# Kernel tuning notes

Hardware: AMD Instinct MI355X
Metric: run time of the kernel (lower is better)

Reference implementation:

```python
import jax, jax.numpy as jnp
import numpy as np

N = 100000
E_RAND = 800000
IN_D, HID_D, OUT_D = 128, 64, 64
PROP_STEP = 8
ATTN_AFT = PROP_STEP // 2  # attention applied after this many prop steps
LAM = 1.0
ALP = 1.0 / (LAM + 1.0)    # alp=0 in init -> DGL auto-sets 1/(lam+1)
TAU = 0.2
P_RHO = 1.0
T_UP = -1.0                # T<=0 -> no upper threshold


def setup_inputs() -> dict:
    key = jax.random.key(0)
    k1, k2, k3, k4, k5 = jax.random.split(key, 5)
    loops = jnp.arange(N)
    src = jnp.concatenate([jax.random.randint(k1, (E_RAND,), 0, N), loops]).astype(jnp.int32)
    dst = jnp.concatenate([jax.random.randint(k2, (E_RAND,), 0, N), loops]).astype(jnp.int32)
    feat = jax.random.normal(k3, (N, IN_D), jnp.float32)
    # xavier_normal init, zero bias (as in MLP.reset_params)
    W_bef = jax.random.normal(k4, (IN_D, HID_D), jnp.float32) * np.float32(np.sqrt(2.0 / (IN_D + HID_D)))
    b_bef = jnp.zeros((HID_D,), jnp.float32)
    W_aft = jax.random.normal(k5, (HID_D, OUT_D), jnp.float32) * np.float32(np.sqrt(2.0 / (HID_D + OUT_D)))
    b_aft = jnp.zeros((OUT_D,), jnp.float32)
    return {"feat": feat, "W_bef": W_bef, "b_bef": b_bef, "W_aft": W_aft, "b_aft": b_aft, "src": src, "dst": dst}


def _ax(src, dst, w, X):
    # Y = A X with per-edge weights: scatter-add of w_e * X[src_e] into dst_e
    return jax.ops.segment_sum(X[src] * w[:, None], dst, num_segments=N)


def _attention(src, dst, Y):
    hs, hd = Y[src], Y[dst]  # [E, d]
    w = jnp.sum(hs * hs, -1) + jnp.sum(hd * hd, -1) - 2.0 * jnp.sum(hs * hd, -1)  # ||h_u - h_v||^2
    w = jax.nn.relu(w) + 1e-7
    w = jnp.power(w, 1.0 - 0.5 * P_RHO)
    w = jnp.maximum(w, TAU)  # lower threshold tau (in-place clamp in torch)
    if T_UP > 0:
        w = jnp.where(w > T_UP, jnp.inf, w)
    w = 1.0 / w + 1e-9
    deg = jax.ops.segment_sum(w, dst, num_segments=N)  # copy_e -> sum per dst node
    return w, deg


def _prop(src, dst, w, deg, Y, X):
    dt = LAM * deg + (1.0 - LAM)
    nrm = jnp.power(dt, -0.5)[:, None]
    py = nrm * _ax(src, dst, w, nrm * Y)
    return (1.0 - ALP) * Y + ALP * LAM * py + ALP * (X / dt[:, None])


def reference(feat, W_bef, b_bef, W_aft, b_aft, src, dst):
    X = feat @ W_bef + b_bef  # mlp_bef: single Linear(input_d, hidden_d)
    w = jnp.ones(src.shape[0], feat.dtype)  # initial edge weights = 1
    deg = jax.ops.segment_sum(w, dst, num_segments=N)  # in-degrees
    Y = X
    for k in range(PROP_STEP):
        Y = _prop(src, dst, w, deg, Y, X)
        if k == ATTN_AFT - 1:
            w, deg = _attention(src, dst, Y)
    # mlp_aft: init_activate=True (relu; norm='none', dropout=0) then Linear(hidden_d, output_d)
    return jax.nn.relu(Y) @ W_aft + b_aft
```

## Files before the change

### kernel.cpp

```cpp
#include <hip/hip_runtime.h>
#include <math.h>

#define IN_D 128
#define HID 64

typedef unsigned short ushort_t;
typedef unsigned int uint_t;

static __device__ __forceinline__ ushort_t f2bf(float f) {
    uint_t x = __float_as_uint(f);
    uint_t r = x + 0x7fffu + ((x >> 16) & 1u);
    return (ushort_t)(r >> 16);
}
static __device__ __forceinline__ float bf2f(ushort_t u) {
    return __uint_as_float(((uint_t)u) << 16);
}


__global__ void zero1_kernel(int* a, int n) {
    int i = blockIdx.x * blockDim.x + threadIdx.x;
    if (i < n) a[i] = 0;
}

__global__ void hist_kernel(const int* __restrict__ dst, int E, int* __restrict__ cnt) {
    int e = blockIdx.x * blockDim.x + threadIdx.x;
    if (e < E) atomicAdd(&cnt[dst[e]], 1);
}

__global__ void scan1_kernel(int* __restrict__ cnt, int N,
                             int* __restrict__ row_ptr, int* __restrict__ blocksum,
                             float* __restrict__ nrm, float* __restrict__ invdt) {
    __shared__ int sm[1024];
    int i = blockIdx.x * 1024 + threadIdx.x;
    int v = (i < N) ? cnt[i] : 0;
    if (i < N) {
        cnt[i] = 0;
        float d = (float)v;
        nrm[i] = 1.0f / sqrtf(d);
        invdt[i] = 1.0f / d;
    }
    sm[threadIdx.x] = v;
    __syncthreads();
    for (int off = 1; off < 1024; off <<= 1) {
        int t = (threadIdx.x >= off) ? sm[threadIdx.x - off] : 0;
        __syncthreads();
        sm[threadIdx.x] += t;
        __syncthreads();
    }
    if (i < N) row_ptr[i + 1] = sm[threadIdx.x];
    if (threadIdx.x == 1023) blocksum[blockIdx.x] = sm[1023];
}

__global__ void scan2_kernel(int* __restrict__ blocksum, int nb) {
    __shared__ int sm[1024];
    int v = (threadIdx.x < nb) ? blocksum[threadIdx.x] : 0;
    sm[threadIdx.x] = v;
    __syncthreads();
    for (int off = 1; off < 1024; off <<= 1) {
        int t = (threadIdx.x >= off) ? sm[threadIdx.x - off] : 0;
        __syncthreads();
        sm[threadIdx.x] += t;
        __syncthreads();
    }
    if (threadIdx.x < nb) blocksum[threadIdx.x] = sm[threadIdx.x] - v;
}

__global__ void scan3_kernel(int* __restrict__ row_ptr, int N, const int* __restrict__ blocksum) {
    int i = blockIdx.x * 1024 + threadIdx.x;
    if (i < N) row_ptr[i + 1] += blocksum[blockIdx.x];
    if (i == 0) row_ptr[0] = 0;
}

__global__ void scatter_kernel(const int* __restrict__ src, const int* __restrict__ dst, int E,
                               const int* __restrict__ row_ptr, int* __restrict__ cursor,
                               const float* __restrict__ nrm,
                               int* __restrict__ src_perm, int* __restrict__ dst_perm,
                               float* __restrict__ coef) {
    int e = blockIdx.x * blockDim.x + threadIdx.x;
    if (e < E) {
        int d = dst[e];
        int s = src[e];
        int pos = row_ptr[d] + atomicAdd(&cursor[d], 1);
        src_perm[pos] = s;
        dst_perm[pos] = d;
        coef[pos] = nrm[s];
    }
}

__global__ void coef_kernel(const int* __restrict__ src_perm, const float* __restrict__ w_perm,
                            const float* __restrict__ nrm, int E, float* __restrict__ coef) {
    int e = blockIdx.x * blockDim.x + threadIdx.x;
    if (e < E) coef[e] = w_perm[e] * nrm[src_perm[e]];
}


__global__ __launch_bounds__(256) void prop_kernel(
    const float* __restrict__ Yin, const ushort_t* __restrict__ Ybf,
    const float* __restrict__ X,
    const int* __restrict__ row_ptr, const int* __restrict__ src_perm,
    const float* __restrict__ coef, const float* __restrict__ nrm,
    const float* __restrict__ invdt, int N,
    float* __restrict__ Yout, ushort_t* __restrict__ Yout_bf) {
    int wave = (blockIdx.x * blockDim.x + threadIdx.x) >> 6;
    int lane = threadIdx.x & 63;
    if (wave >= N) return;
    int r0 = row_ptr[wave], r1 = row_ptr[wave + 1];
    float acc = 0.0f;
    for (int jb = r0; jb < r1; jb += 64) {
        int m = r1 - jb;
        if (m > 64) m = 64;
        int sv = 0;
        float cv = 0.0f;
        if (lane < m) { sv = src_perm[jb + lane]; cv = coef[jb + lane]; }
        for (int t = 0; t < m; t += 16) {
            float v[16], c[16];
            #pragma unroll
            for (int u = 0; u < 16; ++u) {
                int idx = t + u;
                int active = idx < m;
                if (!active) idx = 0;
                int s = __shfl(sv, idx, 64);
                float cc = __shfl(cv, idx, 64);
                c[u] = active ? cc : 0.0f;
                v[u] = bf2f(Ybf[(size_t)s * HID + lane]);
            }
            #pragma unroll
            for (int u = 0; u < 16; ++u) acc = fmaf(c[u], v[u], acc);
        }
    }
    size_t base = (size_t)wave * HID + lane;
    float out = 0.5f * Yin[base] + (0.5f * nrm[wave]) * acc + (0.5f * invdt[wave]) * X[base];
    Yout[base] = out;
    Yout_bf[base] = f2bf(out);
}

__global__ __launch_bounds__(256) void attn_edge_kernel(
    const ushort_t* __restrict__ Ybf,
    const int* __restrict__ src_perm, const int* __restrict__ dst_perm,
    int E, float* __restrict__ w_perm) {
    int e = blockIdx.x * blockDim.x + threadIdx.x;
    if (e >= E) return;
    int s = src_perm[e], d = dst_perm[e];
    const uint4* ps = (const uint4*)(Ybf + (size_t)s * HID);
    const uint4* pd = (const uint4*)(Ybf + (size_t)d * HID);
    uint4 a[8], b[8];
    #pragma unroll
    for (int i = 0; i < 8; ++i) a[i] = ps[i];
    #pragma unroll
    for (int i = 0; i < 8; ++i) b[i] = pd[i];
    float ss = 0.0f;
    #pragma unroll
    for (int i = 0; i < 8; ++i) {
        const uint_t* ua = (const uint_t*)&a[i];
        const uint_t* ub = (const uint_t*)&b[i];
        #pragma unroll
        for (int j = 0; j < 4; ++j) {
            float slo = __uint_as_float(ua[j] << 16);
            float dlo = __uint_as_float(ub[j] << 16);
            float shi = __uint_as_float(ua[j] & 0xffff0000u);
            float dhi = __uint_as_float(ub[j] & 0xffff0000u);
            float t0 = slo - dlo;
            float t1 = shi - dhi;
            ss = fmaf(t0, t0, ss);
            ss = fmaf(t1, t1, ss);
        }
    }
    float w = fmaxf(ss, 0.0f) + 1e-7f;
    w = sqrtf(w);
    w = fmaxf(w, 0.2f);
    w = 1.0f / w + 1e-9f;
    w_perm[e] = w;
}

__global__ __launch_bounds__(256) void deg_sum_kernel(
    const float* __restrict__ w_perm, const int* __restrict__ row_ptr, int N,
    float* __restrict__ nrm, float* __restrict__ invdt) {
    int v = (blockIdx.x * blockDim.x + threadIdx.x) >> 6;
    int lane = threadIdx.x & 63;
    if (v >= N) return;
    int r0 = row_ptr[v], r1 = row_ptr[v + 1];
    float s = 0.0f;
    for (int j = r0 + lane; j < r1; j += 64) s += w_perm[j];
    #pragma unroll
    for (int o = 32; o >= 1; o >>= 1) s += __shfl_xor(s, o, 64);
    if (lane == 0) {
        nrm[v] = 1.0f / sqrtf(s);
        invdt[v] = 1.0f / s;
    }
}

__global__ __launch_bounds__(256) void gemm1_kernel(
    const float* __restrict__ feat, const float* __restrict__ W,
    const float* __restrict__ b, int N, float* __restrict__ X, ushort_t* __restrict__ Xbf) {
    __shared__ float Wl[IN_D * HID];
    __shared__ float featL[8 * IN_D];
    for (int i = threadIdx.x; i < IN_D * HID; i += 256) Wl[i] = W[i];
    int c = threadIdx.x & 63;
    int rsub = threadIdx.x >> 6;
    float bias = b[c];
    int ngroups = N / 8;
    const float4* feat4 = (const float4*)feat;
    for (int g = blockIdx.x; g < ngroups; g += gridDim.x) {
        __syncthreads();
        ((float4*)featL)[threadIdx.x] = feat4[(size_t)g * 256 + threadIdx.x];
        __syncthreads();
        const float4* f0 = (const float4*)&featL[rsub * IN_D];
        const float4* f1 = (const float4*)&featL[(rsub + 4) * IN_D];
        float acc0 = bias, acc1 = bias;
        #pragma unroll
        for (int k4 = 0; k4 < IN_D / 4; ++k4) {
            float4 a = f0[k4];
            float4 e = f1[k4];
            float w0 = Wl[(4 * k4 + 0) * HID + c];
            float w1 = Wl[(4 * k4 + 1) * HID + c];
            float w2 = Wl[(4 * k4 + 2) * HID + c];
            float w3 = Wl[(4 * k4 + 3) * HID + c];
            acc0 += a.x * w0 + a.y * w1 + a.z * w2 + a.w * w3;
            acc1 += e.x * w0 + e.y * w1 + e.z * w2 + e.w * w3;
        }
        size_t row = (size_t)g * 8;
        X[(row + rsub) * HID + c] = acc0;
        X[(row + rsub + 4) * HID + c] = acc1;
        Xbf[(row + rsub) * HID + c] = f2bf(acc0);
        Xbf[(row + rsub + 4) * HID + c] = f2bf(acc1);
    }
}

__global__ __launch_bounds__(256) void gemm2_kernel(
    const float* __restrict__ Y, const float* __restrict__ W,
    const float* __restrict__ b, int N, float* __restrict__ out) {
    __shared__ float Wl[HID * HID];
    __shared__ float Yl[8 * HID];
    for (int i = threadIdx.x; i < HID * HID; i += 256) Wl[i] = W[i];
    int c = threadIdx.x & 63;
    int rsub = threadIdx.x >> 6;
    float bias = b[c];
    int ngroups = N / 8;
    const float4* Y4 = (const float4*)Y;
    for (int g = blockIdx.x; g < ngroups; g += gridDim.x) {
        __syncthreads();
        if (threadIdx.x < 128) {
            float4 v = Y4[(size_t)g * 128 + threadIdx.x];
            v.x = fmaxf(v.x, 0.0f); v.y = fmaxf(v.y, 0.0f);
            v.z = fmaxf(v.z, 0.0f); v.w = fmaxf(v.w, 0.0f);
            ((float4*)Yl)[threadIdx.x] = v;
        }
        __syncthreads();
        const float4* f0 = (const float4*)&Yl[rsub * HID];
        const float4* f1 = (const float4*)&Yl[(rsub + 4) * HID];
        float acc0 = bias, acc1 = bias;
        #pragma unroll
        for (int k4 = 0; k4 < HID / 4; ++k4) {
            float4 a = f0[k4];
            float4 e = f1[k4];
            float w0 = Wl[(4 * k4 + 0) * HID + c];
            float w1 = Wl[(4 * k4 + 1) * HID + c];
            float w2 = Wl[(4 * k4 + 2) * HID + c];
            float w3 = Wl[(4 * k4 + 3) * HID + c];
            acc0 += a.x * w0 + a.y * w1 + a.z * w2 + a.w * w3;
            acc1 += e.x * w0 + e.y * w1 + e.z * w2 + e.w * w3;
        }
        size_t row = (size_t)g * 8;
        out[(row + rsub) * HID + c] = acc0;
        out[(row + rsub + 4) * HID + c] = acc1;
    }
}


extern "C" void kernel_launch(void* const* d_in, const int* in_sizes, int n_in,
                              void* d_out, int out_size, void* d_ws, size_t ws_size,
                              hipStream_t stream) {
    const float* feat  = (const float*)d_in[0];
    const float* W_bef = (const float*)d_in[1];
    const float* b_bef = (const float*)d_in[2];
    const float* W_aft = (const float*)d_in[3];
    const float* b_aft = (const float*)d_in[4];
    const int*   src   = (const int*)d_in[5];
    const int*   dst   = (const int*)d_in[6];

    const int N = in_sizes[0] / IN_D;
    const int E = in_sizes[5];

    char* p = (char*)d_ws;
    auto alloc = [&](size_t bytes) -> void* {
        void* r = (void*)p;
        p += (bytes + 255) & ~(size_t)255;
        return r;
    };
    float*    X       = (float*)alloc((size_t)N * HID * 4);
    float*    Ya      = (float*)alloc((size_t)N * HID * 4);
    float*    Yb      = (float*)alloc((size_t)N * HID * 4);
    ushort_t* Xbf     = (ushort_t*)alloc((size_t)N * HID * 2);
    ushort_t* Yabf    = (ushort_t*)alloc((size_t)N * HID * 2);
    ushort_t* Ybbf    = (ushort_t*)alloc((size_t)N * HID * 2);
    int*      cnt     = (int*)alloc((size_t)N * 4);
    int*      row_ptr = (int*)alloc((size_t)(N + 1) * 4);
    int*      blocksum= (int*)alloc(4096);
    int*      src_perm= (int*)alloc((size_t)E * 4);
    int*      dst_perm= (int*)alloc((size_t)E * 4);
    float*    w_perm  = (float*)alloc((size_t)E * 4);
    float*    coef    = (float*)alloc((size_t)E * 4);
    float*    nrm     = (float*)alloc((size_t)N * 4);
    float*    invdt   = (float*)alloc((size_t)N * 4);

    const int TB = 256;
    dim3 blk(TB);
    int gN   = (N + TB - 1) / TB;
    int gE   = (E + TB - 1) / TB;
    int gNW  = (N * 64 + TB - 1) / TB;
    int nb   = (N + 1023) / 1024;

    zero1_kernel<<<gN, blk, 0, stream>>>(cnt, N);
    hist_kernel<<<gE, blk, 0, stream>>>(dst, E, cnt);
    scan1_kernel<<<nb, 1024, 0, stream>>>(cnt, N, row_ptr, blocksum, nrm, invdt);
    scan2_kernel<<<1, 1024, 0, stream>>>(blocksum, nb);
    scan3_kernel<<<nb, 1024, 0, stream>>>(row_ptr, N, blocksum);
    scatter_kernel<<<gE, blk, 0, stream>>>(src, dst, E, row_ptr, cnt, nrm,
                                           src_perm, dst_perm, coef);

    gemm1_kernel<<<2048, blk, 0, stream>>>(feat, W_bef, b_bef, N, X, Xbf);

    prop_kernel<<<gNW, blk, 0, stream>>>(X,  Xbf,  X, row_ptr, src_perm, coef, nrm, invdt, N, Ya, Yabf);
    prop_kernel<<<gNW, blk, 0, stream>>>(Ya, Yabf, X, row_ptr, src_perm, coef, nrm, invdt, N, Yb, Ybbf);
    prop_kernel<<<gNW, blk, 0, stream>>>(Yb, Ybbf, X, row_ptr, src_perm, coef, nrm, invdt, N, Ya, Yabf);
    prop_kernel<<<gNW, blk, 0, stream>>>(Ya, Yabf, X, row_ptr, src_perm, coef, nrm, invdt, N, Yb, Ybbf);

    attn_edge_kernel<<<gE, blk, 0, stream>>>(Ybbf, src_perm, dst_perm, E, w_perm);
    deg_sum_kernel<<<gNW, blk, 0, stream>>>(w_perm, row_ptr, N, nrm, invdt);
    coef_kernel<<<gE, blk, 0, stream>>>(src_perm, w_perm, nrm, E, coef);

    prop_kernel<<<gNW, blk, 0, stream>>>(Yb, Ybbf, X, row_ptr, src_perm, coef, nrm, invdt, N, Ya, Yabf);
    prop_kernel<<<gNW, blk, 0, stream>>>(Ya, Yabf, X, row_ptr, src_perm, coef, nrm, invdt, N, Yb, Ybbf);
    prop_kernel<<<gNW, blk, 0, stream>>>(Yb, Ybbf, X, row_ptr, src_perm, coef, nrm, invdt, N, Ya, Yabf);
    prop_kernel<<<gNW, blk, 0, stream>>>(Ya, Yabf, X, row_ptr, src_perm, coef, nrm, invdt, N, Yb, Ybbf);

    gemm2_kernel<<<512, blk, 0, stream>>>(Yb, W_aft, b_aft, N, (float*)d_out);
}
```

Baseline: 641.1 us.

## Use scalar edge loads in prop kernel and process 16 rows per GEMM group

```diff
diff --git a/kernel.cpp b/kernel.cpp
--- a/kernel.cpp
+++ b/kernel.cpp
@@ -101,32 +101,37 @@
     const float* __restrict__ coef, const float* __restrict__ nrm,
     const float* __restrict__ invdt, int N,
     float* __restrict__ Yout, ushort_t* __restrict__ Yout_bf) {
-    int wave = (blockIdx.x * blockDim.x + threadIdx.x) >> 6;
+    int wave = __builtin_amdgcn_readfirstlane((blockIdx.x * blockDim.x + threadIdx.x) >> 6);
     int lane = threadIdx.x & 63;
     if (wave >= N) return;
     int r0 = row_ptr[wave], r1 = row_ptr[wave + 1];
     float acc = 0.0f;
-    for (int jb = r0; jb < r1; jb += 64) {
-        int m = r1 - jb;
-        if (m > 64) m = 64;
-        int sv = 0;
-        float cv = 0.0f;
-        if (lane < m) { sv = src_perm[jb + lane]; cv = coef[jb + lane]; }
-        for (int t = 0; t < m; t += 16) {
-            float v[16], c[16];
-            #pragma unroll
-            for (int u = 0; u < 16; ++u) {
-                int idx = t + u;
-                int active = idx < m;
-                if (!active) idx = 0;
-                int s = __shfl(sv, idx, 64);
-                float cc = __shfl(cv, idx, 64);
-                c[u] = active ? cc : 0.0f;
-                v[u] = bf2f(Ybf[(size_t)s * HID + lane]);
-            }
-            #pragma unroll
-            for (int u = 0; u < 16; ++u) acc = fmaf(c[u], v[u], acc);
-        }
+    int j = r0;
+    for (; j + 4 <= r1; j += 4) {
+        float v[4], c[4];
+        #pragma unroll
+        for (int u = 0; u < 4; ++u) {
+            int s = src_perm[j + u];
+            c[u] = coef[j + u];
+            v[u] = bf2f(Ybf[(size_t)s * HID + lane]);
+        }
+        #pragma unroll
+        for (int u = 0; u < 4; ++u) acc = fmaf(c[u], v[u], acc);
+    }
+    if (j < r1) {
+        float v[4], c[4];
+        #pragma unroll
+        for (int u = 0; u < 4; ++u) {
+            int jj = j + u;
+            int valid = jj < r1;
+            int idx = valid ? jj : r1 - 1;
+            int s = src_perm[idx];
+            float cc = coef[idx];
+            c[u] = valid ? cc : 0.0f;
+            v[u] = bf2f(Ybf[(size_t)s * HID + lane]);
+        }
+        #pragma unroll
+        for (int u = 0; u < 4; ++u) acc = fmaf(c[u], v[u], acc);
     }
     size_t base = (size_t)wave * HID + lane;
     float out = 0.5f * Yin[base] + (0.5f * nrm[wave]) * acc + (0.5f * invdt[wave]) * X[base];
@@ -193,36 +198,48 @@
     const float* __restrict__ feat, const float* __restrict__ W,
     const float* __restrict__ b, int N, float* __restrict__ X, ushort_t* __restrict__ Xbf) {
     __shared__ float Wl[IN_D * HID];
-    __shared__ float featL[8 * IN_D];
+    __shared__ float featL[16 * IN_D];
     for (int i = threadIdx.x; i < IN_D * HID; i += 256) Wl[i] = W[i];
     int c = threadIdx.x & 63;
     int rsub = threadIdx.x >> 6;
     float bias = b[c];
-    int ngroups = N / 8;
+    int ngroups = N / 16;
     const float4* feat4 = (const float4*)feat;
     for (int g = blockIdx.x; g < ngroups; g += gridDim.x) {
         __syncthreads();
-        ((float4*)featL)[threadIdx.x] = feat4[(size_t)g * 256 + threadIdx.x];
-        __syncthreads();
-        const float4* f0 = (const float4*)&featL[rsub * IN_D];
+        float4* fl4 = (float4*)featL;
+        fl4[threadIdx.x]       = feat4[(size_t)g * 512 + threadIdx.x];
+        fl4[threadIdx.x + 256] = feat4[(size_t)g * 512 + 256 + threadIdx.x];
+        __syncthreads();
+        const float4* f0 = (const float4*)&featL[(rsub) * IN_D];
         const float4* f1 = (const float4*)&featL[(rsub + 4) * IN_D];
-        float acc0 = bias, acc1 = bias;
+        const float4* f2 = (const float4*)&featL[(rsub + 8) * IN_D];
+        const float4* f3 = (const float4*)&featL[(rsub + 12) * IN_D];
+        float acc0 = bias, acc1 = bias, acc2 = bias, acc3 = bias;
         #pragma unroll
         for (int k4 = 0; k4 < IN_D / 4; ++k4) {
             float4 a = f0[k4];
             float4 e = f1[k4];
+            float4 h = f2[k4];
+            float4 q = f3[k4];
             float w0 = Wl[(4 * k4 + 0) * HID + c];
             float w1 = Wl[(4 * k4 + 1) * HID + c];
             float w2 = Wl[(4 * k4 + 2) * HID + c];
             float w3 = Wl[(4 * k4 + 3) * HID + c];
             acc0 += a.x * w0 + a.y * w1 + a.z * w2 + a.w * w3;
             acc1 += e.x * w0 + e.y * w1 + e.z * w2 + e.w * w3;
-        }
-        size_t row = (size_t)g * 8;
+            acc2 += h.x * w0 + h.y * w1 + h.z * w2 + h.w * w3;
+            acc3 += q.x * w0 + q.y * w1 + q.z * w2 + q.w * w3;
+        }
+        size_t row = (size_t)g * 16;
         X[(row + rsub) * HID + c] = acc0;
         X[(row + rsub + 4) * HID + c] = acc1;
+        X[(row + rsub + 8) * HID + c] = acc2;
+        X[(row + rsub + 12) * HID + c] = acc3;
         Xbf[(row + rsub) * HID + c] = f2bf(acc0);
         Xbf[(row + rsub + 4) * HID + c] = f2bf(acc1);
+        Xbf[(row + rsub + 8) * HID + c] = f2bf(acc2);
+        Xbf[(row + rsub + 12) * HID + c] = f2bf(acc3);
     }
 }
 
@@ -230,39 +247,47 @@
     const float* __restrict__ Y, const float* __restrict__ W,
     const float* __restrict__ b, int N, float* __restrict__ out) {
     __shared__ float Wl[HID * HID];
-    __shared__ float Yl[8 * HID];
+    __shared__ float Yl[16 * HID];
     for (int i = threadIdx.x; i < HID * HID; i += 256) Wl[i] = W[i];
     int c = threadIdx.x & 63;
     int rsub = threadIdx.x >> 6;
     float bias = b[c];
-    int ngroups = N / 8;
+    int ngroups = N / 16;
     const float4* Y4 = (const float4*)Y;
     for (int g = blockIdx.x; g < ngroups; g += gridDim.x) {
         __syncthreads();
-        if (threadIdx.x < 128) {
-            float4 v = Y4[(size_t)g * 128 + threadIdx.x];
+        {
+            float4 v = Y4[(size_t)g * 256 + threadIdx.x];
             v.x = fmaxf(v.x, 0.0f); v.y = fmaxf(v.y, 0.0f);
             v.z = fmaxf(v.z, 0.0f); v.w = fmaxf(v.w, 0.0f);
             ((float4*)Yl)[threadIdx.x] = v;
         }
         __syncthreads();
-        const float4* f0 = (const float4*)&Yl[rsub * HID];
+        const float4* f0 = (const float4*)&Yl[(rsub) * HID];
         const float4* f1 = (const float4*)&Yl[(rsub + 4) * HID];
-        float acc0 = bias, acc1 = bias;
+        const float4* f2 = (const float4*)&Yl[(rsub + 8) * HID];
+        const float4* f3 = (const float4*)&Yl[(rsub + 12) * HID];
+        float acc0 = bias, acc1 = bias, acc2 = bias, acc3 = bias;
         #pragma unroll
         for (int k4 = 0; k4 < HID / 4; ++k4) {
             float4 a = f0[k4];
             float4 e = f1[k4];
+            float4 h = f2[k4];
+            float4 q = f3[k4];
             float w0 = Wl[(4 * k4 + 0) * HID + c];
             float w1 = Wl[(4 * k4 + 1) * HID + c];
             float w2 = Wl[(4 * k4 + 2) * HID + c];
             float w3 = Wl[(4 * k4 + 3) * HID + c];
             acc0 += a.x * w0 + a.y * w1 + a.z * w2 + a.w * w3;
             acc1 += e.x * w0 + e.y * w1 + e.z * w2 + e.w * w3;
-        }
-        size_t row = (size_t)g * 8;
+            acc2 += h.x * w0 + h.y * w1 + h.z * w2 + h.w * w3;
+            acc3 += q.x * w0 + q.y * w1 + q.z * w2 + q.w * w3;
+        }
+        size_t row = (size_t)g * 16;
         out[(row + rsub) * HID + c] = acc0;
         out[(row + rsub + 4) * HID + c] = acc1;
+        out[(row + rsub + 8) * HID + c] = acc2;
+        out[(row + rsub + 12) * HID + c] = acc3;
     }
 }
 
```

Result: faster. 615.3 us (-4.0%).
